# Kernel optimization log

Hardware: AMD Instinct MI355X
Metric: run time of the kernel (lower is better)

## Reference

```python
import jax, jax.numpy as jnp
import numpy as np
import math


def _dfrtmtrx(Npts, a):
    # Faithful to torch dfrtmtrx: Evec = I, so einsum('ij,jk,ni->nk', f, I, I) == f,
    # i.e. F = sqrt(N) * diag(exp(-1j*pi/2 * a * l)) with l = [0..N-2, N-1+even].
    even = 1 - Npts % 2
    l = jnp.arange(Npts).at[-1].add(even)            # last entry is N-1+even
    diag = jnp.exp((-1j) * (math.pi / 2) * a * l)     # complex64 when a is float32
    return (Npts ** 0.5) * jnp.diag(diag)             # [Npts, Npts] complex64


def setup_inputs() -> dict:
    key = jax.random.key(0)
    k1, k2 = jax.random.split(key)
    x = jax.random.normal(k1, (8, 64, 256, 256), dtype=jnp.float32)
    order = jax.random.normal(k2, (1,), dtype=jnp.float32)  # nn.Parameter(torch.randn(1))
    return {"x": x, "order": order}


def reference(x, order):
    N, C, H, W = x.shape
    a = order[0]
    Fh = _dfrtmtrx(H, a)  # [H, H] complex64
    Fw = _dfrtmtrx(W, a)  # [W, W] complex64
    xs = jnp.fft.fftshift(x, axes=(2, 3)).astype(jnp.complex64)
    # torch broadcasts h_test/w_test over (N, C) via repeat_interleave; plain
    # broadcasting in the einsum is the same math without materializing copies.
    out = jnp.einsum('hk,nckw->nchw', Fh, xs)   # left transform along H
    out = jnp.einsum('nchw,wk->nchk', out, Fw)  # right transform along W
    return jnp.fft.fftshift(out, axes=(2, 3))
```

## Files before the change

### kernel.cpp

```cpp
#include <hip/hip_runtime.h>


constexpr int HW = 256;
constexpr int TOTAL = 8 * 64 * 256 * 256;

__global__ __launch_bounds__(256) void frft_diag_kernel(
    const float* __restrict__ x,
    const float* __restrict__ order,
    float* __restrict__ out,
    int interleaved,
    int nvec)
{
    __shared__ float tc[HW];
    __shared__ float ts[HW];

    const int t = threadIdx.x;
    {
        const int idx = t ^ 128;
        const double l = (idx == 255) ? 256.0 : (double)idx;
        const double theta = 1.5707963267948966 * (double)order[0] * l;
        double s, c;
        sincos(theta, &s, &c);
        tc[t] = (float)(16.0 * c);
        ts[t] = (float)(16.0 * s);
    }
    __syncthreads();

    const float4* __restrict__ xv4 = (const float4*)x;
    float4* __restrict__ ov4 = (float4*)out;

    for (int v = blockIdx.x * blockDim.x + t; v < nvec; v += gridDim.x * blockDim.x) {
        const float4 xv = xv4[v];
        const int base = v << 2;
        const int w0 = base & (HW - 1);
        const int h  = (base >> 8) & (HW - 1);

        const float ch = tc[h];
        const float sh = ts[h];

        const float xs[4] = {xv.x, xv.y, xv.z, xv.w};
        float re[4], im[4];
        #pragma unroll
        for (int j = 0; j < 4; ++j) {
            const float cw = tc[w0 + j];
            const float sw = ts[w0 + j];
            const float pr = ch * cw - sh * sw;
            const float pi = ch * sw + sh * cw;
            re[j] =  xs[j] * pr;
            im[j] = -xs[j] * pi;
        }

        if (interleaved) {
            float4 o0 = {re[0], im[0], re[1], im[1]};
            float4 o1 = {re[2], im[2], re[3], im[3]};
            ov4[2 * v]     = o0;
            ov4[2 * v + 1] = o1;
        } else {
            float4 o = {re[0], re[1], re[2], re[3]};
            ov4[v] = o;
        }
    }
}

extern "C" void kernel_launch(void* const* d_in, const int* in_sizes, int n_in,
                              void* d_out, int out_size, void* d_ws, size_t ws_size,
                              hipStream_t stream) {
    const float* x     = (const float*)d_in[0];
    const float* order = (const float*)d_in[1];
    float* out = (float*)d_out;

    const int total = in_sizes[0];
    const int nvec  = total / 4;
    const int interleaved = (out_size >= 2 * total) ? 1 : 0;

    const int block = 256;
    const int grid  = 2048;
    frft_diag_kernel<<<grid, block, 0, stream>>>(x, order, out, interleaved, nvec);
}
```

Measured before the change: 234.5 us.

## Replace grid-stride loop with one-float2-per-thread full grid launch

Switches from a fixed 2048-block grid-stride loop processing float4 per iteration to a full grid where each thread handles one float2 and writes one float4 of complex output. This aims to increase memory-level parallelism and occupancy for a bandwidth-bound elementwise kernel. The trade-off is that every block recomputes the 256-entry double-precision sincos table, which now happens across many more blocks.

```diff
diff --git a/kernel.cpp b/kernel.cpp
--- a/kernel.cpp
+++ b/kernel.cpp
@@ -2,14 +2,13 @@
 
 
 constexpr int HW = 256;
-constexpr int TOTAL = 8 * 64 * 256 * 256;
 
 __global__ __launch_bounds__(256) void frft_diag_kernel(
     const float* __restrict__ x,
     const float* __restrict__ order,
     float* __restrict__ out,
     int interleaved,
-    int nvec)
+    int nvec2)
 {
     __shared__ float tc[HW];
     __shared__ float ts[HW];
@@ -26,39 +25,29 @@
     }
     __syncthreads();
 
-    const float4* __restrict__ xv4 = (const float4*)x;
-    float4* __restrict__ ov4 = (float4*)out;
+    const int p = blockIdx.x * blockDim.x + t;
+    if (p >= nvec2) return;
 
-    for (int v = blockIdx.x * blockDim.x + t; v < nvec; v += gridDim.x * blockDim.x) {
-        const float4 xv = xv4[v];
-        const int base = v << 2;
-        const int w0 = base & (HW - 1);
-        const int h  = (base >> 8) & (HW - 1);
+    const float2 xv = ((const float2*)x)[p];
+    const int e  = p << 1;
+    const int w0 = e & (HW - 1);
+    const int h  = (e >> 8) & (HW - 1);
 
-        const float ch = tc[h];
-        const float sh = ts[h];
+    const float ch = tc[h],      sh = ts[h];
+    const float c0 = tc[w0],     s0 = ts[w0];
+    const float c1 = tc[w0 + 1], s1 = ts[w0 + 1];
 
-        const float xs[4] = {xv.x, xv.y, xv.z, xv.w};
-        float re[4], im[4];
-        #pragma unroll
-        for (int j = 0; j < 4; ++j) {
-            const float cw = tc[w0 + j];
-            const float sw = ts[w0 + j];
-            const float pr = ch * cw - sh * sw;
-            const float pi = ch * sw + sh * cw;
-            re[j] =  xs[j] * pr;
-            im[j] = -xs[j] * pi;
-        }
+    const float pr0 = ch * c0 - sh * s0;
+    const float pi0 = ch * s0 + sh * c0;
+    const float pr1 = ch * c1 - sh * s1;
+    const float pi1 = ch * s1 + sh * c1;
 
-        if (interleaved) {
-            float4 o0 = {re[0], im[0], re[1], im[1]};
-            float4 o1 = {re[2], im[2], re[3], im[3]};
-            ov4[2 * v]     = o0;
-            ov4[2 * v + 1] = o1;
-        } else {
-            float4 o = {re[0], re[1], re[2], re[3]};
-            ov4[v] = o;
-        }
+    if (interleaved) {
+        float4 o = { xv.x * pr0, -xv.x * pi0, xv.y * pr1, -xv.y * pi1 };
+        ((float4*)out)[p] = o;
+    } else {
+        float2 o = { xv.x * pr0, xv.y * pr1 };
+        ((float2*)out)[p] = o;
     }
 }
 
@@ -70,10 +59,10 @@
     float* out = (float*)d_out;
 
     const int total = in_sizes[0];
-    const int nvec  = total / 4;
+    const int nvec2 = total / 2;
     const int interleaved = (out_size >= 2 * total) ? 1 : 0;
 
     const int block = 256;
-    const int grid  = 2048;
-    frft_diag_kernel<<<grid, block, 0, stream>>>(x, order, out, interleaved, nvec);
+    const int grid  = (nvec2 + block - 1) / block;
+    frft_diag_kernel<<<grid, block, 0, stream>>>(x, order, out, interleaved, nvec2);
 }
```

Result: faster. 227.6 us (-2.9%).
